# Performance work log

Measured on AMD Instinct MI355X. Metric: run time of the kernel, lower is better.

## Reference

```python
import jax, jax.numpy as jnp
import numpy as np

DIM = 768
NUM_HEADS = 12
WH, WW = 14, 14
N_TOK = WH * WW + 1  # 197, includes CLS token
NUM_REL_DIST = (2 * WH - 1) * (2 * WW - 1) + 3  # 732
HEAD_DIM = DIM // NUM_HEADS
SCALE = HEAD_DIM ** -0.5


def _relative_position_index():
    # Mirrors the torch buffer construction (constant, int).
    coords = np.stack(np.meshgrid(np.arange(WH), np.arange(WW), indexing='ij'))  # [2,WH,WW]
    cf = coords.reshape(2, -1)  # [2, WH*WW]
    rel = cf[:, :, None] - cf[:, None, :]  # [2, N, N]
    rel = rel.transpose(1, 2, 0).astype(np.int64)
    rel[:, :, 0] += WH - 1
    rel[:, :, 1] += WW - 1
    rel[:, :, 0] *= 2 * WW - 1
    idx = np.zeros((N_TOK, N_TOK), dtype=np.int64)
    idx[1:, 1:] = rel.sum(-1)
    idx[0, 0:] = NUM_REL_DIST - 3
    idx[0:, 0] = NUM_REL_DIST - 2
    idx[0, 0] = NUM_REL_DIST - 1
    return jnp.asarray(idx)

REL_POS_INDEX = _relative_position_index()


def setup_inputs() -> dict:
    key = jax.random.key(0)
    ks = jax.random.split(key, 7)
    B = 64
    x = jax.random.normal(ks[0], (B, N_TOK, DIM), dtype=jnp.float32)
    qkv_weight = jax.random.normal(ks[1], (3 * DIM, DIM), dtype=jnp.float32) * 0.02
    q_bias = jax.random.normal(ks[2], (DIM,), dtype=jnp.float32) * 0.02
    v_bias = jax.random.normal(ks[3], (DIM,), dtype=jnp.float32) * 0.02
    rel_pos_bias_table = jax.random.normal(ks[4], (NUM_REL_DIST, NUM_HEADS), dtype=jnp.float32) * 0.02
    proj_weight = jax.random.normal(ks[5], (DIM, DIM), dtype=jnp.float32) * 0.02
    proj_bias = jax.random.normal(ks[6], (DIM,), dtype=jnp.float32) * 0.02
    return {"x": x, "qkv_weight": qkv_weight, "q_bias": q_bias, "v_bias": v_bias,
            "rel_pos_bias_table": rel_pos_bias_table, "proj_weight": proj_weight,
            "proj_bias": proj_bias}


def reference(x, qkv_weight, q_bias, v_bias, rel_pos_bias_table, proj_weight, proj_bias):
    B, N, C = x.shape
    qkv_bias = jnp.concatenate([q_bias, jnp.zeros_like(v_bias), v_bias])
    qkv = x @ qkv_weight.T + qkv_bias  # [B, N, 3C]
    qkv = qkv.reshape(B, N, 3, NUM_HEADS, HEAD_DIM).transpose(2, 0, 3, 1, 4)
    q, k, v = qkv[0], qkv[1], qkv[2]  # each [B, H, N, D]
    attn = jnp.einsum('bhnd,bhmd->bhnm', q * SCALE, k)  # [B, H, N, N]
    rpb = rel_pos_bias_table[REL_POS_INDEX]  # [N, N, H]
    attn = attn + rpb.transpose(2, 0, 1)[None]  # [1, H, N, N]
    attn = jax.nn.softmax(attn, axis=-1)
    out = jnp.einsum('bhnm,bhmd->bhnd', attn, v)  # [B, H, N, D]
    out = out.transpose(0, 2, 1, 3).reshape(B, N, C)
    return out @ proj_weight.T + proj_bias
```

## Files before the change

kernel.cpp:

```cpp
#include <hip/hip_runtime.h>
#include <hip/hip_bf16.h>

#define DIM 768
#define QKVD 2304
#define NHEADS 12
#define NTOK 197
#define NP 208
#define NPS 232
#define M_ROWS 12608
#define M_PAD 12800
#define HEADS_TOT 768
#define NT 24

typedef __attribute__((ext_vector_type(8))) short bf16x8;
typedef __attribute__((ext_vector_type(4))) float f32x4;

__device__ inline short f2bf(float f) {
  union { __hip_bfloat16 h; short s; } u;
  u.h = __float2bfloat16(f);
  return u.s;
}

__device__ __forceinline__ void gload16(const short* g, short* l) {
  __builtin_amdgcn_global_load_lds((const __attribute__((address_space(1))) void*)g,
                                   (__attribute__((address_space(3))) void*)l, 16, 0, 0);
}

__device__ __forceinline__ int xcd_swz(int orig, int nwg) {
  int q = nwg >> 3, r = nwg & 7;
  int x = orig & 7, p = orig >> 3;
  return (x < r ? x * (q + 1) : r * (q + 1) + (x - r) * q) + p;
}

__global__ void convert_kernel(const float* __restrict__ x, const float* __restrict__ wq,
                               const float* __restrict__ wp,
                               short* __restrict__ xb, short* __restrict__ wqb,
                               short* __restrict__ wpb) {
  int idx = blockIdx.x * 256 + threadIdx.x;
  const int n_x  = M_ROWS * DIM / 4;
  const int n_wq = 3 * DIM * DIM / 4;
  const int n_wp = DIM * DIM / 4;
  const int n_pad = (M_PAD - M_ROWS) * DIM / 4;
  if (idx >= n_x + n_wq + n_wp) {
    int k = idx - n_x - n_wq - n_wp;
    if (k < n_pad) {
      short4 z = {0, 0, 0, 0};
      *(short4*)(xb + (size_t)M_ROWS * DIM + (size_t)k * 4) = z;
    }
    return;
  }
  const float4* src; short* dst; int off;
  if (idx < n_x)             { src = (const float4*)x;  dst = xb;  off = idx; }
  else if (idx < n_x + n_wq) { src = (const float4*)wq; dst = wqb; off = idx - n_x; }
  else                       { src = (const float4*)wp; dst = wpb; off = idx - n_x - n_wq; }
  float4 v = src[off];
  short4 o;
  o.x = f2bf(v.x); o.y = f2bf(v.y); o.z = f2bf(v.z); o.w = f2bf(v.w);
  *(short4*)(dst + (size_t)off * 4) = o;
}

__global__ void rpb_kernel(const float* __restrict__ table, float* __restrict__ rpbf) {
  int idx = blockIdx.x * 256 + threadIdx.x;
  const int tot = NHEADS * NP * NP;
  if (idx >= tot) return;
  int h = idx / (NP * NP);
  int rem = idx - h * NP * NP;
  int i = rem / NP;
  int j = rem - i * NP;
  float v = 0.f;
  if (i < NTOK && j < NTOK) {
    int t;
    if (i == 0 && j == 0) t = 731;
    else if (i == 0)      t = 729;
    else if (j == 0)      t = 730;
    else {
      int p = i - 1, q = j - 1;
      int ri = p / 14, ci = p - ri * 14;
      int rj = q / 14, cj = q - rj * 14;
      t = (ri - rj + 13) * 27 + (ci - cj + 13);
    }
    v = table[t * NHEADS + h];
  }
  rpbf[idx] = v;
}

template<bool DOSTAGE>
__device__ __forceinline__ void ktile256(int kt, short* lds,
                                         const short* Asrc, const short* Bsrc, short* sdst,
                                         int aoff, int boff, f32x4 (&acc)[8][4]) {
  short* base = lds + (kt & 3) * 16384;
  const short* Ab = base + aoff;
  const short* Bb = base + boff;
  short* stg = sdst + ((kt + 3) & 3) * 16384;
  const int kc = (kt + 3) * 32;
  bf16x8 bfr[4];
#pragma unroll
  for (int j = 0; j < 4; ++j) bfr[j] = *(const bf16x8*)(Bb + j * 512);
  {
    if (DOSTAGE) {
      gload16(Asrc + kc, stg);
      gload16(Bsrc + kc, stg + 8192);
    }
    bf16x8 af[4];
#pragma unroll
    for (int j = 0; j < 4; ++j) af[j] = *(const bf16x8*)(Ab + j * 512);
    __builtin_amdgcn_s_barrier();
    __builtin_amdgcn_s_setprio(1);
#pragma unroll
    for (int j = 0; j < 4; ++j)
#pragma unroll
      for (int n = 0; n < 4; ++n)
        acc[j][n] = __builtin_amdgcn_mfma_f32_16x16x32_bf16(af[j], bfr[n], acc[j][n], 0, 0, 0);
    __builtin_amdgcn_s_setprio(0);
  }
  __builtin_amdgcn_s_barrier();
  {
    if (DOSTAGE) {
      gload16(Asrc + (size_t)128 * DIM + kc, stg + 4096);
      gload16(Bsrc + (size_t)128 * DIM + kc, stg + 8192 + 4096);
    }
    bf16x8 af[4];
#pragma unroll
    for (int j = 0; j < 4; ++j) af[j] = *(const bf16x8*)(Ab + 2048 + j * 512);
    __builtin_amdgcn_s_barrier();
    __builtin_amdgcn_s_setprio(1);
#pragma unroll
    for (int j = 0; j < 4; ++j)
#pragma unroll
      for (int n = 0; n < 4; ++n)
        acc[4 + j][n] = __builtin_amdgcn_mfma_f32_16x16x32_bf16(af[j], bfr[n], acc[4 + j][n], 0, 0, 0);
    __builtin_amdgcn_s_setprio(0);
  }
}

__device__ __forceinline__ void gemm256_mainloop(const short* __restrict__ A,
                                                 const short* __restrict__ Bw,
                                                 int tm, int tn, short* lds, f32x4 (&acc)[8][4]) {
  const int tid = threadIdx.x;
  const int srow = tid >> 2;
  const int sslot = ((tid & 3) - (tid >> 3)) & 3;
  const int l = tid & 63, lr = l & 15, lg = l >> 4;
  const int w = tid >> 6, wm = w >> 2, wn = w & 3;
  const short* Asrc = A + (size_t)(tm * 256 + srow) * DIM + sslot * 8;
  const short* Bsrc = Bw + (size_t)(tn * 256 + srow) * DIM + sslot * 8;
  short* sdst = lds + tid * 8;
  const int slotR = (lg + (lr >> 1)) & 3;
  const int aoff = wm * 4096 + lr * 32 + slotR * 8;
  const int boff = 8192 + (wn >> 1) * 4096 + ((wn & 1) * 64 + lr) * 32 + slotR * 8;
#pragma unroll
  for (int m = 0; m < 8; ++m)
#pragma unroll
    for (int n = 0; n < 4; ++n) { f32x4 z = {0.f, 0.f, 0.f, 0.f}; acc[m][n] = z; }

#pragma unroll
  for (int kt = 0; kt < 3; ++kt) {
    gload16(Asrc + kt * 32, sdst + kt * 16384);
    gload16(Bsrc + kt * 32, sdst + kt * 16384 + 8192);
    gload16(Asrc + (size_t)128 * DIM + kt * 32, sdst + kt * 16384 + 4096);
    gload16(Bsrc + (size_t)128 * DIM + kt * 32, sdst + kt * 16384 + 8192 + 4096);
  }
  asm volatile("s_waitcnt vmcnt(8)" ::: "memory");
  __builtin_amdgcn_s_barrier();

  for (int kt = 0; kt < NT - 3; ++kt) {
    ktile256<true>(kt, lds, Asrc, Bsrc, sdst, aoff, boff, acc);
    asm volatile("s_waitcnt vmcnt(8)" ::: "memory");
    __builtin_amdgcn_s_barrier();
  }
  ktile256<false>(NT - 3, lds, Asrc, Bsrc, sdst, aoff, boff, acc);
  asm volatile("s_waitcnt vmcnt(4)" ::: "memory");
  __builtin_amdgcn_s_barrier();
  ktile256<false>(NT - 2, lds, Asrc, Bsrc, sdst, aoff, boff, acc);
  asm volatile("s_waitcnt vmcnt(0)" ::: "memory");
  __builtin_amdgcn_s_barrier();
  ktile256<false>(NT - 1, lds, Asrc, Bsrc, sdst, aoff, boff, acc);
}

__global__ __launch_bounds__(512)
void gemm_qkv_kernel(const short* __restrict__ xb, const short* __restrict__ wqb,
                     const float* __restrict__ q_bias, const float* __restrict__ v_bias,
                     short* __restrict__ qkvb) {
  __shared__ __attribute__((aligned(16))) short lds[65536];
  const int wg = xcd_swz(blockIdx.x, 50 * 9);
  const int tn = wg % 9, tm = wg / 9;
  f32x4 acc[8][4];
  gemm256_mainloop(xb, wqb, tm, tn, lds, acc);

  const int tid = threadIdx.x;
  const int w = tid >> 6, wm = w >> 2, wn = w & 3;
  const int l = tid & 63, lr = l & 15, lg = l >> 4;
  const int rbase = tm * 256 + wm * 128, cbase = tn * 256 + wn * 64;
#pragma unroll
  for (int n = 0; n < 4; ++n) {
    int c = cbase + n * 16 + lr;
    int part = (c < 768) ? 0 : ((c < 1536) ? 1 : 2);
    float bias = (part == 0) ? q_bias[c] : ((part == 2) ? v_bias[c - 1536] : 0.f);
    float scl = (part == 0) ? 0.125f : 1.f;
#pragma unroll
    for (int m = 0; m < 8; ++m) {
#pragma unroll
      for (int i = 0; i < 4; ++i) {
        int r = rbase + m * 16 + lg * 4 + i;
        qkvb[(size_t)r * QKVD + c] = f2bf((acc[m][n][i] + bias) * scl);
      }
    }
  }
}

__device__ inline void gemm_tile_mainloop128(const short* __restrict__ A, const short* __restrict__ Bw,
                                             int tm, int tn,
                                             short* As0, short* Bs0, short* As1, short* Bs1,
                                             f32x4 (&acc)[4][4]) {
  const int tid = threadIdx.x;
  const int l = tid & 63, lr = l & 15, lg = l >> 4;
  const int w = tid >> 6, wm = w >> 1, wn = w & 1;
  const int row = tid >> 2;
  const int c8 = (((tid & 3) ^ ((tid >> 3) & 3)) << 3);
  const int rs = (((lg ^ ((lr >> 1) & 3))) << 3);
  const short* Ag = A + (size_t)(tm * 128 + row) * DIM + c8;
  const short* Bg = Bw + (size_t)(tn * 128 + row) * DIM + c8;
  const int dOff = tid * 8;
#pragma unroll
  for (int m = 0; m < 4; ++m)
#pragma unroll
    for (int n = 0; n < 4; ++n) { f32x4 z = {0.f, 0.f, 0.f, 0.f}; acc[m][n] = z; }

  gload16(Ag, As0 + dOff);
  gload16(Ag + (size_t)64 * DIM, As0 + 2048 + dOff);
  gload16(Bg, Bs0 + dOff);
  gload16(Bg + (size_t)64 * DIM, Bs0 + 2048 + dOff);
  __syncthreads();

  for (int kt = 0; kt < NT; ++kt) {
    short* Ac = (kt & 1) ? As1 : As0;
    short* Bc = (kt & 1) ? Bs1 : Bs0;
    short* An = (kt & 1) ? As0 : As1;
    short* Bn = (kt & 1) ? Bs0 : Bs1;
    if (kt < NT - 1) {
      gload16(Ag + (kt + 1) * 32, An + dOff);
      gload16(Ag + (size_t)64 * DIM + (kt + 1) * 32, An + 2048 + dOff);
      gload16(Bg + (kt + 1) * 32, Bn + dOff);
      gload16(Bg + (size_t)64 * DIM + (kt + 1) * 32, Bn + 2048 + dOff);
    }
    bf16x8 af[4], bfr[4];
#pragma unroll
    for (int m = 0; m < 4; ++m)
      af[m] = *(const bf16x8*)(Ac + (wm * 64 + m * 16 + lr) * 32 + rs);
#pragma unroll
    for (int n = 0; n < 4; ++n)
      bfr[n] = *(const bf16x8*)(Bc + (wn * 64 + n * 16 + lr) * 32 + rs);
#pragma unroll
    for (int m = 0; m < 4; ++m)
#pragma unroll
      for (int n = 0; n < 4; ++n)
        acc[m][n] = __builtin_amdgcn_mfma_f32_16x16x32_bf16(af[m], bfr[n], acc[m][n], 0, 0, 0);
    __syncthreads();
  }
}

__global__ __launch_bounds__(512, 1)
void attn_kernel(const short* __restrict__ qkvb, const float* __restrict__ rpbf,
                 short* __restrict__ aout) {
  __shared__ __attribute__((aligned(16))) short Klds[208 * 64];
  __shared__ __attribute__((aligned(16))) short Vlds[64 * NPS];
  __shared__ __attribute__((aligned(16))) short Plds[8 * 16 * NPS];
  const int bh = blockIdx.x;
  const int b = bh / 12, h = bh - b * 12;
  const short* base = qkvb + (size_t)(b * 197) * QKVD;
  const short* Qg = base + h * 64;
  const short* Kg = base + 768 + h * 64;
  const short* Vg = base + 1536 + h * 64;
  const float* RP = rpbf + (size_t)h * NP * NP;
  const int tid = threadIdx.x;
  const int wave = tid >> 6, l = tid & 63, lr = l & 15, lg = l >> 4;

  for (int c = tid; c < 1664; c += 512) {
    int r = c >> 3, sp = c & 7;
    int rr = r < NTOK ? r : NTOK - 1;
    gload16(Kg + (size_t)rr * QKVD + ((sp ^ (r & 7)) << 3), Klds + c * 8);
  }
  for (int idx = tid; idx < 64 * NP; idx += 512) {
    int t = idx >> 6, d = idx & 63;
    int tt = t < NTOK ? t : NTOK - 1;
    Vlds[d * NPS + t] = Vg[(size_t)tt * QKVD + d];
  }
  __syncthreads();
  if (tid < 64) {
    for (int j = NP; j < NPS; ++j) Vlds[tid * NPS + j] = 0;
  }
  __syncthreads();

  short* Pw = Plds + wave * 16 * NPS;
  for (int s = wave; s < 13; s += 8) {
    const int row0 = s * 16;
    const int qrow = (row0 + lr < NTOK) ? (row0 + lr) : (NTOK - 1);
    bf16x8 qf0 = *(const bf16x8*)(Qg + (size_t)qrow * QKVD + lg * 8);
    bf16x8 qf1 = *(const bf16x8*)(Qg + (size_t)qrow * QKVD + 32 + lg * 8);
    f32x4 acc[13];
#pragma unroll
    for (int t = 0; t < 13; ++t) { f32x4 z = {0.f, 0.f, 0.f, 0.f}; acc[t] = z; }
    __builtin_amdgcn_s_setprio(1);
#pragma unroll
    for (int t = 0; t < 13; ++t) {
      int rk = t * 16 + lr;
      int sw = lr & 7;
      bf16x8 kf0 = *(const bf16x8*)(Klds + rk * 64 + ((lg ^ sw) << 3));
      bf16x8 kf1 = *(const bf16x8*)(Klds + rk * 64 + (((4 + lg) ^ sw) << 3));
      acc[t] = __builtin_amdgcn_mfma_f32_16x16x32_bf16(qf0, kf0, acc[t], 0, 0, 0);
      acc[t] = __builtin_amdgcn_mfma_f32_16x16x32_bf16(qf1, kf1, acc[t], 0, 0, 0);
    }
    __builtin_amdgcn_s_setprio(0);
    float sum4[4];
#pragma unroll
    for (int i = 0; i < 4; ++i) {
      const int row = row0 + lg * 4 + i;
      const float* rp = RP + (size_t)row * NP;
      float sv[13];
      float mx = -3e38f;
#pragma unroll
      for (int t = 0; t < 13; ++t) {
        int col = t * 16 + lr;
        float s_ = (col < NTOK) ? (acc[t][i] + rp[col]) : -3e38f;
        sv[t] = s_;
        mx = fmaxf(mx, s_);
      }
      mx = fmaxf(mx, __shfl_xor(mx, 1, 16));
      mx = fmaxf(mx, __shfl_xor(mx, 2, 16));
      mx = fmaxf(mx, __shfl_xor(mx, 4, 16));
      mx = fmaxf(mx, __shfl_xor(mx, 8, 16));
      float sm = 0.f;
#pragma unroll
      for (int t = 0; t < 13; ++t) {
        float p = __expf(sv[t] - mx);
        sm += p;
        Pw[(lg * 4 + i) * NPS + t * 16 + lr] = f2bf(p);
      }
      sm += __shfl_xor(sm, 1, 16);
      sm += __shfl_xor(sm, 2, 16);
      sm += __shfl_xor(sm, 4, 16);
      sm += __shfl_xor(sm, 8, 16);
      sum4[i] = sm;
      Pw[(lg * 4 + i) * NPS + 208 + lr] = 0;
    }
    f32x4 o[4];
#pragma unroll
    for (int dt = 0; dt < 4; ++dt) { f32x4 z = {0.f, 0.f, 0.f, 0.f}; o[dt] = z; }
    __builtin_amdgcn_s_setprio(1);
#pragma unroll
    for (int jb = 0; jb < 7; ++jb) {
      bf16x8 pf = *(const bf16x8*)(Pw + lr * NPS + jb * 32 + lg * 8);
#pragma unroll
      for (int dt = 0; dt < 4; ++dt) {
        bf16x8 vf = *(const bf16x8*)(Vlds + (dt * 16 + lr) * NPS + jb * 32 + lg * 8);
        o[dt] = __builtin_amdgcn_mfma_f32_16x16x32_bf16(pf, vf, o[dt], 0, 0, 0);
      }
    }
    __builtin_amdgcn_s_setprio(0);
#pragma unroll
    for (int i = 0; i < 4; ++i) {
      const int row = row0 + lg * 4 + i;
      if (row < NTOK) {
        float inv = 1.f / sum4[i];
        size_t base2 = (size_t)(b * 197 + row) * DIM + h * 64;
#pragma unroll
        for (int dt = 0; dt < 4; ++dt)
          aout[base2 + dt * 16 + lr] = f2bf(o[dt][i] * inv);
      }
    }
  }
}

__global__ void gemm_proj_kernel(const short* __restrict__ ab, const short* __restrict__ wpb,
                                 const float* __restrict__ proj_bias, float* __restrict__ out) {
  __shared__ __attribute__((aligned(16))) short As0[128 * 32];
  __shared__ __attribute__((aligned(16))) short Bs0[128 * 32];
  __shared__ __attribute__((aligned(16))) short As1[128 * 32];
  __shared__ __attribute__((aligned(16))) short Bs1[128 * 32];
  const int wg = xcd_swz(blockIdx.x, 99 * 6);
  const int tn = wg % 6, tm = wg / 6;
  f32x4 acc[4][4];
  gemm_tile_mainloop128(ab, wpb, tm, tn, As0, Bs0, As1, Bs1, acc);

  const int tid = threadIdx.x;
  const int w = tid >> 6, l = tid & 63, lr = l & 15, lg = l >> 4;
  const int wm = w >> 1, wn = w & 1;
  const int rbase = tm * 128 + wm * 64, cbase = tn * 128 + wn * 64;
#pragma unroll
  for (int n = 0; n < 4; ++n) {
    int c = cbase + n * 16 + lr;
    float pb = proj_bias[c];
#pragma unroll
    for (int m = 0; m < 4; ++m) {
#pragma unroll
      for (int i = 0; i < 4; ++i) {
        int r = rbase + m * 16 + lg * 4 + i;
        if (r < M_ROWS) out[(size_t)r * DIM + c] = acc[m][n][i] + pb;
      }
    }
  }
}

extern "C" void kernel_launch(void* const* d_in, const int* in_sizes, int n_in,
                              void* d_out, int out_size, void* d_ws, size_t ws_size,
                              hipStream_t stream) {
  const float* x         = (const float*)d_in[0];
  const float* wqkv      = (const float*)d_in[1];
  const float* q_bias    = (const float*)d_in[2];
  const float* v_bias    = (const float*)d_in[3];
  const float* table     = (const float*)d_in[4];
  const float* wproj     = (const float*)d_in[5];
  const float* proj_bias = (const float*)d_in[6];
  float* out = (float*)d_out;

  char* p = (char*)d_ws;
  short* xb    = (short*)p; p += (size_t)M_PAD * DIM * 2;
  short* wqb   = (short*)p; p += (size_t)3 * DIM * DIM * 2;
  short* wpb   = (short*)p; p += (size_t)DIM * DIM * 2;
  short* qkvb  = (short*)p; p += (size_t)M_PAD * QKVD * 2;
  float* rpbf  = (float*)p; p += (size_t)NHEADS * NP * NP * 4;
  short* aout  = xb;

  const int conv_tot = (M_ROWS * DIM + 3 * DIM * DIM + DIM * DIM + (M_PAD - M_ROWS) * DIM) / 4;
  convert_kernel<<<(conv_tot + 255) / 256, 256, 0, stream>>>(x, wqkv, wproj, xb, wqb, wpb);
  rpb_kernel<<<(NHEADS * NP * NP + 255) / 256, 256, 0, stream>>>(table, rpbf);
  gemm_qkv_kernel<<<50 * 9, 512, 0, stream>>>(xb, wqb, q_bias, v_bias, qkvb);
  attn_kernel<<<HEADS_TOT, 512, 0, stream>>>(qkvb, rpbf, aout);
  gemm_proj_kernel<<<99 * 6, 256, 0, stream>>>(aout, wpb, proj_bias, out);
}
```

Before: 149.6 us.

## Double-buffer LDS fragments in registers and cut barriers in GEMM mainloop

Restructures the 256x256 bf16 GEMM main loop so each k-tile step computes on fragments already held in registers. While it does that, it loads the next tile's A/B fragments from LDS into a second register set, alternating two sets across unrolled step pairs. The three barriers per tile become a single barrier with adjusted vmcnt waits, to overlap LDS reads with MFMA work and cut sync stalls. The QKV kernel also gets a launch-bounds hint of two blocks per CU. That hint, together with the extra fragment registers, risks register pressure or spills, and the 128 KB LDS per block may not allow a second block anyway.

```diff
diff --git a/kernel.cpp b/kernel.cpp
--- a/kernel.cpp
+++ b/kernel.cpp
@@ -84,53 +84,48 @@
   rpbf[idx] = v;
 }
 
-template<bool DOSTAGE>
-__device__ __forceinline__ void ktile256(int kt, short* lds,
-                                         const short* Asrc, const short* Bsrc, short* sdst,
-                                         int aoff, int boff, f32x4 (&acc)[8][4]) {
-  short* base = lds + (kt & 3) * 16384;
-  const short* Ab = base + aoff;
-  const short* Bb = base + boff;
-  short* stg = sdst + ((kt + 3) & 3) * 16384;
+
+__device__ __forceinline__ void tile_step(int kt, short* lds,
+                                          const short* Asrc, const short* Bsrc, short* sdst,
+                                          int aoff, int boff,
+                                          bf16x8 (&afc)[8], bf16x8 (&bfc)[4],
+                                          bf16x8 (&afn)[8], bf16x8 (&bfn)[4],
+                                          f32x4 (&acc)[8][4]) {
+  const bool stg = (kt < NT - 3);
+  const bool pre = (kt < NT - 1);
+  const short* nb = lds + ((kt + 1) & 3) * 16384;
+  short* stgd = sdst + ((kt + 3) & 3) * 16384;
   const int kc = (kt + 3) * 32;
-  bf16x8 bfr[4];
-#pragma unroll
-  for (int j = 0; j < 4; ++j) bfr[j] = *(const bf16x8*)(Bb + j * 512);
-  {
-    if (DOSTAGE) {
-      gload16(Asrc + kc, stg);
-      gload16(Bsrc + kc, stg + 8192);
-    }
-    bf16x8 af[4];
-#pragma unroll
-    for (int j = 0; j < 4; ++j) af[j] = *(const bf16x8*)(Ab + j * 512);
-    __builtin_amdgcn_s_barrier();
-    __builtin_amdgcn_s_setprio(1);
-#pragma unroll
-    for (int j = 0; j < 4; ++j)
-#pragma unroll
-      for (int n = 0; n < 4; ++n)
-        acc[j][n] = __builtin_amdgcn_mfma_f32_16x16x32_bf16(af[j], bfr[n], acc[j][n], 0, 0, 0);
-    __builtin_amdgcn_s_setprio(0);
-  }
+  if (stg) { gload16(Asrc + kc, stgd); gload16(Bsrc + kc, stgd + 8192); }
+  if (pre) {
+#pragma unroll
+    for (int n = 0; n < 4; ++n) bfn[n] = *(const bf16x8*)(nb + boff + n * 512);
+#pragma unroll
+    for (int j = 0; j < 4; ++j) afn[j] = *(const bf16x8*)(nb + aoff + j * 512);
+  }
+  __builtin_amdgcn_s_setprio(1);
+#pragma unroll
+  for (int j = 0; j < 4; ++j)
+#pragma unroll
+    for (int n = 0; n < 4; ++n)
+      acc[j][n] = __builtin_amdgcn_mfma_f32_16x16x32_bf16(afc[j], bfc[n], acc[j][n], 0, 0, 0);
+  __builtin_amdgcn_s_setprio(0);
+  if (stg) { gload16(Asrc + (size_t)128 * DIM + kc, stgd + 4096);
+             gload16(Bsrc + (size_t)128 * DIM + kc, stgd + 8192 + 4096); }
+  if (pre) {
+#pragma unroll
+    for (int j = 0; j < 4; ++j) afn[4 + j] = *(const bf16x8*)(nb + aoff + 2048 + j * 512);
+  }
+  __builtin_amdgcn_s_setprio(1);
+#pragma unroll
+  for (int j = 0; j < 4; ++j)
+#pragma unroll
+    for (int n = 0; n < 4; ++n)
+      acc[4 + j][n] = __builtin_amdgcn_mfma_f32_16x16x32_bf16(afc[4 + j], bfc[n], acc[4 + j][n], 0, 0, 0);
+  __builtin_amdgcn_s_setprio(0);
+  if (kt < NT - 3)       { asm volatile("s_waitcnt vmcnt(4)" ::: "memory"); }
+  else if (kt == NT - 3) { asm volatile("s_waitcnt vmcnt(0)" ::: "memory"); }
   __builtin_amdgcn_s_barrier();
-  {
-    if (DOSTAGE) {
-      gload16(Asrc + (size_t)128 * DIM + kc, stg + 4096);
-      gload16(Bsrc + (size_t)128 * DIM + kc, stg + 8192 + 4096);
-    }
-    bf16x8 af[4];
-#pragma unroll
-    for (int j = 0; j < 4; ++j) af[j] = *(const bf16x8*)(Ab + 2048 + j * 512);
-    __builtin_amdgcn_s_barrier();
-    __builtin_amdgcn_s_setprio(1);
-#pragma unroll
-    for (int j = 0; j < 4; ++j)
-#pragma unroll
-      for (int n = 0; n < 4; ++n)
-        acc[4 + j][n] = __builtin_amdgcn_mfma_f32_16x16x32_bf16(af[j], bfr[n], acc[4 + j][n], 0, 0, 0);
-    __builtin_amdgcn_s_setprio(0);
-  }
 }
 
 __device__ __forceinline__ void gemm256_mainloop(const short* __restrict__ A,
@@ -159,24 +154,24 @@
     gload16(Asrc + (size_t)128 * DIM + kt * 32, sdst + kt * 16384 + 4096);
     gload16(Bsrc + (size_t)128 * DIM + kt * 32, sdst + kt * 16384 + 8192 + 4096);
   }
-  asm volatile("s_waitcnt vmcnt(8)" ::: "memory");
-  __builtin_amdgcn_s_barrier();
-
-  for (int kt = 0; kt < NT - 3; ++kt) {
-    ktile256<true>(kt, lds, Asrc, Bsrc, sdst, aoff, boff, acc);
-    asm volatile("s_waitcnt vmcnt(8)" ::: "memory");
-    __builtin_amdgcn_s_barrier();
-  }
-  ktile256<false>(NT - 3, lds, Asrc, Bsrc, sdst, aoff, boff, acc);
   asm volatile("s_waitcnt vmcnt(4)" ::: "memory");
   __builtin_amdgcn_s_barrier();
-  ktile256<false>(NT - 2, lds, Asrc, Bsrc, sdst, aoff, boff, acc);
-  asm volatile("s_waitcnt vmcnt(0)" ::: "memory");
-  __builtin_amdgcn_s_barrier();
-  ktile256<false>(NT - 1, lds, Asrc, Bsrc, sdst, aoff, boff, acc);
-}
-
-__global__ __launch_bounds__(512)
+
+  bf16x8 afA[8], bfA[4], afB[8], bfB[4];
+#pragma unroll
+  for (int n = 0; n < 4; ++n) bfA[n] = *(const bf16x8*)(lds + boff + n * 512);
+#pragma unroll
+  for (int j = 0; j < 4; ++j) afA[j] = *(const bf16x8*)(lds + aoff + j * 512);
+#pragma unroll
+  for (int j = 0; j < 4; ++j) afA[4 + j] = *(const bf16x8*)(lds + aoff + 2048 + j * 512);
+
+  for (int kt = 0; kt < NT; kt += 2) {
+    tile_step(kt,     lds, Asrc, Bsrc, sdst, aoff, boff, afA, bfA, afB, bfB, acc);
+    tile_step(kt + 1, lds, Asrc, Bsrc, sdst, aoff, boff, afB, bfB, afA, bfA, acc);
+  }
+}
+
+__global__ __launch_bounds__(512, 2)
 void gemm_qkv_kernel(const short* __restrict__ xb, const short* __restrict__ wqb,
                      const float* __restrict__ q_bias, const float* __restrict__ v_bias,
                      short* __restrict__ qkvb) {
```

Result: no change. 148.4 us (-0.8%).
